# Kernel optimization log

Measured on AMD Instinct MI355X. Metric: run time of the kernel, lower is better.

The kernel has to match this reference:

```python
import jax, jax.numpy as jnp
import numpy as np

TIME_CONSTANT = 1.0
VM_THRESHOLD = 2.0
WINDOW = 100          # integration_window
AMPLITUDE = 1.0


def setup_inputs() -> dict:
    key = jax.random.key(0)
    # [B, T, H, W, C] positive drive so integrate-and-fire actually spikes
    inputs = jax.random.uniform(key, (4, 200, 64, 64, 8), dtype=jnp.float32)
    return {"inputs": inputs}


def _process_chunk(chunk):
    """Iterative integrate-and-fire on one time chunk [B, T, H, W, C].
    Each while-iteration extracts one spike per neuron (first threshold
    crossing of the running cumsum), resets the membrane, and zeroes the
    consumed input so the next cumsum restarts after the spike."""
    B, T = chunk.shape[0], chunk.shape[1]
    img = chunk.shape[2:]
    spikes0 = jnp.zeros((B,) + img + (T + 1,), chunk.dtype)
    vout0 = jnp.zeros_like(chunk)

    def body(state):
        ch, vout, spikes, _ = state
        V = jnp.cumsum(ch * TIME_CONSTANT, axis=1)            # membrane potential
        temp = jax.nn.relu(V - VM_THRESHOLD)
        has = jnp.any(temp > 0)                                # any neuron fires?
        ctemp = jnp.cumsum(temp, axis=1)                       # zero before first crossing
        tstar = jnp.sum((ctemp == 0).astype(jnp.int32), axis=1)  # [B,H,W,C] spike time (T => none)
        spikes_new = spikes + jax.nn.one_hot(tstar, T + 1, dtype=ch.dtype)
        rolled = jnp.roll(ctemp, 1, axis=1).at[:, 0].set(0.0)  # nonzero strictly after spike
        mask = rolled == 0
        vout_spk = jnp.where(mask, vout + V, 0.0)              # record V up to spike, reset after
        ch_spk = jnp.where(mask, 0.0, ch)                      # consume input up to spike
        # if no spikes this pass: accumulate residual V and stop (do-while break)
        vout_n = jnp.where(has, vout_spk, vout + V)
        ch_n = jnp.where(has, ch_spk, ch)
        spikes_n = jnp.where(has, spikes_new, spikes)
        return ch_n, vout_n, spikes_n, jnp.logical_not(has)

    def cond(state):
        return jnp.logical_not(state[3])

    state = (chunk, vout0, spikes0, jnp.array(False))
    _, vout, spikes, _ = jax.lax.while_loop(cond, body, state)
    return vout, spikes[..., :T]   # drop the 'no spike' bin


def reference(inputs):
    T = inputs.shape[1]
    sizes = [WINDOW] * (T // WINDOW) + ([T % WINDOW] if T % WINDOW else [])
    spike_chunks = []
    start = 0
    for s in sizes:  # small fixed chunk loop (structural, not a data dim)
        ch = inputs[:, start:start + s]
        start += s
        _, sp = _process_chunk(ch)
        spike_chunks.append(sp)
    spikes = jnp.concatenate(spike_chunks, axis=-1)   # [B, H, W, C, T]
    out = jnp.swapaxes(spikes, 1, -1)                 # [B, T, W, C, H] (as in source)
    if AMPLITUDE != 1.0:
        out = out * AMPLITUDE
    return out
```

## Files before the change

kernel.cpp:

```cpp
#include <hip/hip_runtime.h>
#include <stdint.h>

#define HWC   32768
#define TTOT  200
#define CHUNK 100

__global__ __launch_bounds__(256) void spike_fused(const float* __restrict__ x,
                                                   float* __restrict__ out) {
    __shared__ uint32_t lds[4 * 544];

    unsigned bid  = blockIdx.x;
    unsigned slab = bid >> 6;
    unsigned hh   = (bid >> 5) & 1u;
    unsigned tile = bid & 31u;
    unsigned b    = slab >> 1, ch = slab & 1u;
    unsigned h0   = hh * 32u;
    unsigned wc0  = tile * 16u;
    unsigned tid  = threadIdx.x;

    {
        unsigned hl = tid >> 3;
        unsigned wq = tid & 7u;
        unsigned n  = (h0 + hl) * 512u + wc0 + wq * 2u;
        const float2* xp = (const float2*)x
            + (((size_t)(b * TTOT + ch * CHUNK) * HWC + n) >> 1);

        float a0 = 0.0f, a1 = 0.0f;
        uint32_t wa[4] = {0u, 0u, 0u, 0u};
        uint32_t wb[4] = {0u, 0u, 0u, 0u};

#define STEP(TW, BB, K)                                                     \
    do {                                                                    \
        a0 += v[K].x;                                                       \
        if (a0 > 2.0f) { wa[TW] |= (1u << ((BB) + (K))); a0 = 0.0f; }       \
        a1 += v[K].y;                                                       \
        if (a1 > 2.0f) { wb[TW] |= (1u << ((BB) + (K))); a1 = 0.0f; }       \
    } while (0)

#define GROUP8(TW, TBASE)                                                   \
    do {                                                                    \
        float2 v[8];                                                        \
        _Pragma("unroll")                                                   \
        for (int k = 0; k < 8; ++k)                                         \
            v[k] = xp[(size_t)((TBASE) + k) * (HWC / 2)];                   \
        STEP(TW, (TBASE) & 31, 0); STEP(TW, (TBASE) & 31, 1);               \
        STEP(TW, (TBASE) & 31, 2); STEP(TW, (TBASE) & 31, 3);               \
        STEP(TW, (TBASE) & 31, 4); STEP(TW, (TBASE) & 31, 5);               \
        STEP(TW, (TBASE) & 31, 6); STEP(TW, (TBASE) & 31, 7);               \
    } while (0)

        GROUP8(0,  0); GROUP8(0,  8); GROUP8(0, 16); GROUP8(0, 24);
        GROUP8(1, 32); GROUP8(1, 40); GROUP8(1, 48); GROUP8(1, 56);
        GROUP8(2, 64); GROUP8(2, 72); GROUP8(2, 80); GROUP8(2, 88);
        {
            float2 v[4];
#pragma unroll
            for (int k = 0; k < 4; ++k)
                v[k] = xp[(size_t)(96 + k) * (HWC / 2)];
            STEP(3, 0, 0); STEP(3, 0, 1); STEP(3, 0, 2); STEP(3, 0, 3);
        }
#undef GROUP8
#undef STEP

        unsigned lbase = hl * 17u + wq * 2u;
#pragma unroll
        for (int tw = 0; tw < 4; ++tw) {
            lds[tw * 544u + lbase]      = wa[tw];
            lds[tw * 544u + lbase + 1u] = wb[tw];
        }
    }
    __syncthreads();

    unsigned idx  = tid & 127u;
    unsigned half = tid >> 7;
    unsigned wcl  = idx >> 3;
    unsigned hl4  = (idx & 7u) * 4u;

    uint32_t r[4][4];
#pragma unroll
    for (int k = 0; k < 4; ++k)
#pragma unroll
        for (int tw = 0; tw < 4; ++tw)
            r[k][tw] = lds[tw * 544u + (hl4 + k) * 17u + wcl];

    unsigned rbase = b * TTOT + ch * CHUNK;
    size_t   cbase = (size_t)(wc0 + wcl) * 16u + ((h0 + hl4) >> 2);
    float4*  o4    = (float4*)out;

#pragma unroll
    for (int tw = 0; tw < 4; ++tw) {
        const int nj = (tw < 3) ? 16 : 2;
        for (int j = 0; j < nj; ++j) {
            unsigned bit = 2u * (unsigned)j + half;
            unsigned t   = (unsigned)tw * 32u + bit;
            float4 v;
            v.x = (float)((r[0][tw] >> bit) & 1u);
            v.y = (float)((r[1][tw] >> bit) & 1u);
            v.z = (float)((r[2][tw] >> bit) & 1u);
            v.w = (float)((r[3][tw] >> bit) & 1u);
            o4[((size_t)(rbase + t) << 13) + cbase] = v;
        }
    }
}

extern "C" void kernel_launch(void* const* d_in, const int* in_sizes, int n_in,
                              void* d_out, int out_size, void* d_ws, size_t ws_size,
                              hipStream_t stream) {
    (void)in_sizes; (void)n_in; (void)out_size; (void)d_ws; (void)ws_size;
    const float* x = (const float*)d_in[0];
    float* out = (float*)d_out;
    hipLaunchKernelGGL(spike_fused, dim3(512), dim3(256), 0, stream, x, out);
}
```

Measured before the change: 195.1 us.

## Use one neuron per thread with 512-thread blocks and double-buffered loads

The block grows from 256 to 512 threads, and each thread now integrates a single neuron with scalar loads instead of two neurons with float2 loads. Input loads are issued in 16-step groups into two alternating register buffers, so the next group's loads are in flight while the current group's threshold scan runs. The store phase is remapped so four thread groups split the time bits. The goal is more memory parallelism and shorter serial dependency chains in what looks like a latency-bound kernel, at the cost of narrower loads and more registers per thread.

```diff
diff --git a/kernel.cpp b/kernel.cpp
--- a/kernel.cpp
+++ b/kernel.cpp
@@ -5,8 +5,8 @@
 #define TTOT  200
 #define CHUNK 100
 
-__global__ __launch_bounds__(256) void spike_fused(const float* __restrict__ x,
-                                                   float* __restrict__ out) {
+__global__ __launch_bounds__(512, 4) void spike_fused(const float* __restrict__ x,
+                                                      float* __restrict__ out) {
     __shared__ uint32_t lds[4 * 544];
 
     unsigned bid  = blockIdx.x;
@@ -19,79 +19,86 @@
     unsigned tid  = threadIdx.x;
 
     {
-        unsigned hl = tid >> 3;
-        unsigned wq = tid & 7u;
-        unsigned n  = (h0 + hl) * 512u + wc0 + wq * 2u;
-        const float2* xp = (const float2*)x
-            + (((size_t)(b * TTOT + ch * CHUNK) * HWC + n) >> 1);
+        unsigned hl  = tid >> 4;
+        unsigned wcl = tid & 15u;
+        unsigned n   = (h0 + hl) * 512u + wc0 + wcl;
+        const float* xp = x + (size_t)(b * TTOT + ch * CHUNK) * HWC + n;
 
-        float a0 = 0.0f, a1 = 0.0f;
-        uint32_t wa[4] = {0u, 0u, 0u, 0u};
-        uint32_t wb[4] = {0u, 0u, 0u, 0u};
+        float acc = 0.0f;
+        uint32_t w[4] = {0u, 0u, 0u, 0u};
+        float A[16], B[16], Tl[4];
 
-#define STEP(TW, BB, K)                                                     \
+#define LOAD16(V, TBASE)                                                    \
     do {                                                                    \
-        a0 += v[K].x;                                                       \
-        if (a0 > 2.0f) { wa[TW] |= (1u << ((BB) + (K))); a0 = 0.0f; }       \
-        a1 += v[K].y;                                                       \
-        if (a1 > 2.0f) { wb[TW] |= (1u << ((BB) + (K))); a1 = 0.0f; }       \
+        _Pragma("unroll")                                                   \
+        for (int k = 0; k < 16; ++k)                                        \
+            V[k] = xp[(size_t)((TBASE) + k) * HWC];                         \
     } while (0)
 
-#define GROUP8(TW, TBASE)                                                   \
+#define CONS16(V, TBASE)                                                    \
     do {                                                                    \
-        float2 v[8];                                                        \
         _Pragma("unroll")                                                   \
-        for (int k = 0; k < 8; ++k)                                         \
-            v[k] = xp[(size_t)((TBASE) + k) * (HWC / 2)];                   \
-        STEP(TW, (TBASE) & 31, 0); STEP(TW, (TBASE) & 31, 1);               \
-        STEP(TW, (TBASE) & 31, 2); STEP(TW, (TBASE) & 31, 3);               \
-        STEP(TW, (TBASE) & 31, 4); STEP(TW, (TBASE) & 31, 5);               \
-        STEP(TW, (TBASE) & 31, 6); STEP(TW, (TBASE) & 31, 7);               \
+        for (int k = 0; k < 16; ++k) {                                      \
+            acc += V[k];                                                    \
+            if (acc > 2.0f) {                                               \
+                w[(TBASE) >> 5] |= (1u << (((TBASE) & 31) + k));            \
+                acc = 0.0f;                                                 \
+            }                                                               \
+        }                                                                   \
     } while (0)
 
-        GROUP8(0,  0); GROUP8(0,  8); GROUP8(0, 16); GROUP8(0, 24);
-        GROUP8(1, 32); GROUP8(1, 40); GROUP8(1, 48); GROUP8(1, 56);
-        GROUP8(2, 64); GROUP8(2, 72); GROUP8(2, 80); GROUP8(2, 88);
+        LOAD16(A, 0);
+        LOAD16(B, 16);
+        CONS16(A, 0);
+        LOAD16(A, 32);
+        CONS16(B, 16);
+        LOAD16(B, 48);
+        CONS16(A, 32);
+        LOAD16(A, 64);
+        CONS16(B, 48);
+        LOAD16(B, 80);
+        CONS16(A, 64);
         {
-            float2 v[4];
 #pragma unroll
             for (int k = 0; k < 4; ++k)
-                v[k] = xp[(size_t)(96 + k) * (HWC / 2)];
-            STEP(3, 0, 0); STEP(3, 0, 1); STEP(3, 0, 2); STEP(3, 0, 3);
+                Tl[k] = xp[(size_t)(96 + k) * HWC];
         }
-#undef GROUP8
-#undef STEP
+        CONS16(B, 80);
+#pragma unroll
+        for (int k = 0; k < 4; ++k) {
+            acc += Tl[k];
+            if (acc > 2.0f) { w[3] |= (1u << k); acc = 0.0f; }
+        }
+#undef LOAD16
+#undef CONS16
 
-        unsigned lbase = hl * 17u + wq * 2u;
+        unsigned lbase = hl * 17u + wcl;
 #pragma unroll
-        for (int tw = 0; tw < 4; ++tw) {
-            lds[tw * 544u + lbase]      = wa[tw];
-            lds[tw * 544u + lbase + 1u] = wb[tw];
-        }
+        for (int tw = 0; tw < 4; ++tw)
+            lds[tw * 544u + lbase] = w[tw];
     }
     __syncthreads();
 
     unsigned idx  = tid & 127u;
     unsigned half = tid >> 7;
     unsigned wcl  = idx >> 3;
-    unsigned hl4  = (idx & 7u) * 4u;
+    unsigned h4   = (idx & 7u) * 4u;
 
     uint32_t r[4][4];
 #pragma unroll
     for (int k = 0; k < 4; ++k)
 #pragma unroll
         for (int tw = 0; tw < 4; ++tw)
-            r[k][tw] = lds[tw * 544u + (hl4 + k) * 17u + wcl];
+            r[k][tw] = lds[tw * 544u + (h4 + k) * 17u + wcl];
 
     unsigned rbase = b * TTOT + ch * CHUNK;
-    size_t   cbase = (size_t)(wc0 + wcl) * 16u + ((h0 + hl4) >> 2);
+    size_t   cbase = (size_t)(wc0 + wcl) * 16u + ((h0 + h4) >> 2);
     float4*  o4    = (float4*)out;
 
 #pragma unroll
-    for (int tw = 0; tw < 4; ++tw) {
-        const int nj = (tw < 3) ? 16 : 2;
-        for (int j = 0; j < nj; ++j) {
-            unsigned bit = 2u * (unsigned)j + half;
+    for (int tw = 0; tw < 3; ++tw) {
+        for (int j = 0; j < 8; ++j) {
+            unsigned bit = 4u * (unsigned)j + half;
             unsigned t   = (unsigned)tw * 32u + bit;
             float4 v;
             v.x = (float)((r[0][tw] >> bit) & 1u);
@@ -101,6 +108,16 @@
             o4[((size_t)(rbase + t) << 13) + cbase] = v;
         }
     }
+    {
+        unsigned bit = half;
+        unsigned t   = 96u + bit;
+        float4 v;
+        v.x = (float)((r[0][3] >> bit) & 1u);
+        v.y = (float)((r[1][3] >> bit) & 1u);
+        v.z = (float)((r[2][3] >> bit) & 1u);
+        v.w = (float)((r[3][3] >> bit) & 1u);
+        o4[((size_t)(rbase + t) << 13) + cbase] = v;
+    }
 }
 
 extern "C" void kernel_launch(void* const* d_in, const int* in_sizes, int n_in,
@@ -109,5 +126,5 @@
     (void)in_sizes; (void)n_in; (void)out_size; (void)d_ws; (void)ws_size;
     const float* x = (const float*)d_in[0];
     float* out = (float*)d_out;
-    hipLaunchKernelGGL(spike_fused, dim3(512), dim3(256), 0, stream, x, out);
+    hipLaunchKernelGGL(spike_fused, dim3(512), dim3(512), 0, stream, x, out);
 }
```

Result: no change. 194.9 us (-0.1%).

## Pipeline spike scan with transposed stores in 32-step phases per block

Applied to the files above, without the earlier changes.

Restructures the fused kernel so each block covers the full 64 H rows for a 16-wide W*C tile, with 256 blocks instead of 512. Time is processed in 32-step phases: while scanning the next phase's inputs, each thread writes the previous phase's spike bits as transposed float4 outputs, exchanging bitmasks through a small LDS buffer. The goal is to overlap input loads with output stores rather than doing all reads and then all writes. The cost is extra barriers, scalar (non-vectorized) loads, and half as many blocks, which may reduce occupancy.

```diff
diff --git a/kernel.cpp b/kernel.cpp
--- a/kernel.cpp
+++ b/kernel.cpp
@@ -5,102 +5,106 @@
 #define TTOT  200
 #define CHUNK 100
 
-__global__ __launch_bounds__(256) void spike_fused(const float* __restrict__ x,
-                                                   float* __restrict__ out) {
-    __shared__ uint32_t lds[4 * 544];
+__global__ __launch_bounds__(256) void spike_pipe(const float* __restrict__ x,
+                                                  float* __restrict__ out) {
+    __shared__ uint32_t bits[64 * 17];
 
     unsigned bid  = blockIdx.x;
-    unsigned slab = bid >> 6;
-    unsigned hh   = (bid >> 5) & 1u;
-    unsigned tile = bid & 31u;
+    unsigned slab = bid & 7u;
+    unsigned wcT  = bid >> 3;
+    unsigned wc0  = wcT * 16u;
     unsigned b    = slab >> 1, ch = slab & 1u;
-    unsigned h0   = hh * 32u;
-    unsigned wc0  = tile * 16u;
     unsigned tid  = threadIdx.x;
 
-    {
-        unsigned hl = tid >> 3;
-        unsigned wq = tid & 7u;
-        unsigned n  = (h0 + hl) * 512u + wc0 + wq * 2u;
-        const float2* xp = (const float2*)x
-            + (((size_t)(b * TTOT + ch * CHUNK) * HWC + n) >> 1);
+    unsigned wcl  = tid & 15u;
+    unsigned hloc = tid >> 4;
+    const float* xb = x + (size_t)(b * TTOT + ch * CHUNK) * HWC
+                    + (size_t)(hloc * 4u) * 512u + wc0 + wcl;
 
-        float a0 = 0.0f, a1 = 0.0f;
-        uint32_t wa[4] = {0u, 0u, 0u, 0u};
-        uint32_t wb[4] = {0u, 0u, 0u, 0u};
+    unsigned wcs  = tid >> 4;
+    unsigned h0s  = (tid & 15u) * 4u;
+    unsigned rbase = b * TTOT + ch * CHUNK;
+    float4*  o4   = (float4*)out;
+    size_t   cidx = (((size_t)(wc0 + wcs) * 64u) + h0s) >> 2;
 
-#define STEP(TW, BB, K)                                                     \
+    float    a0 = 0.f, a1 = 0.f, a2 = 0.f, a3 = 0.f;
+    uint32_t w0 = 0u, w1 = 0u, w2 = 0u, w3 = 0u;
+    uint32_t r0 = 0u, r1 = 0u, r2 = 0u, r3 = 0u;
+
+#define SCAN(T, J)                                                          \
     do {                                                                    \
-        a0 += v[K].x;                                                       \
-        if (a0 > 2.0f) { wa[TW] |= (1u << ((BB) + (K))); a0 = 0.0f; }       \
-        a1 += v[K].y;                                                       \
-        if (a1 > 2.0f) { wb[TW] |= (1u << ((BB) + (K))); a1 = 0.0f; }       \
+        float v0 = xb[(size_t)(T) * HWC];                                   \
+        float v1 = xb[(size_t)(T) * HWC + 512u];                            \
+        float v2 = xb[(size_t)(T) * HWC + 1024u];                           \
+        float v3 = xb[(size_t)(T) * HWC + 1536u];                           \
+        a0 += v0; if (a0 > 2.0f) { w0 |= 1u << (J); a0 = 0.0f; }            \
+        a1 += v1; if (a1 > 2.0f) { w1 |= 1u << (J); a1 = 0.0f; }            \
+        a2 += v2; if (a2 > 2.0f) { w2 |= 1u << (J); a2 = 0.0f; }            \
+        a3 += v3; if (a3 > 2.0f) { w3 |= 1u << (J); a3 = 0.0f; }            \
     } while (0)
 
-#define GROUP8(TW, TBASE)                                                   \
+#define STASH()                                                             \
     do {                                                                    \
-        float2 v[8];                                                        \
-        _Pragma("unroll")                                                   \
-        for (int k = 0; k < 8; ++k)                                         \
-            v[k] = xp[(size_t)((TBASE) + k) * (HWC / 2)];                   \
-        STEP(TW, (TBASE) & 31, 0); STEP(TW, (TBASE) & 31, 1);               \
-        STEP(TW, (TBASE) & 31, 2); STEP(TW, (TBASE) & 31, 3);               \
-        STEP(TW, (TBASE) & 31, 4); STEP(TW, (TBASE) & 31, 5);               \
-        STEP(TW, (TBASE) & 31, 6); STEP(TW, (TBASE) & 31, 7);               \
+        bits[(hloc * 4u + 0u) * 17u + wcl] = w0;                            \
+        bits[(hloc * 4u + 1u) * 17u + wcl] = w1;                            \
+        bits[(hloc * 4u + 2u) * 17u + wcl] = w2;                            \
+        bits[(hloc * 4u + 3u) * 17u + wcl] = w3;                            \
+        w0 = w1 = w2 = w3 = 0u;                                             \
     } while (0)
 
-        GROUP8(0,  0); GROUP8(0,  8); GROUP8(0, 16); GROUP8(0, 24);
-        GROUP8(1, 32); GROUP8(1, 40); GROUP8(1, 48); GROUP8(1, 56);
-        GROUP8(2, 64); GROUP8(2, 72); GROUP8(2, 80); GROUP8(2, 88);
-        {
-            float2 v[4];
-#pragma unroll
-            for (int k = 0; k < 4; ++k)
-                v[k] = xp[(size_t)(96 + k) * (HWC / 2)];
-            STEP(3, 0, 0); STEP(3, 0, 1); STEP(3, 0, 2); STEP(3, 0, 3);
-        }
-#undef GROUP8
-#undef STEP
+#define HOIST()                                                             \
+    do {                                                                    \
+        r0 = bits[(h0s + 0u) * 17u + wcs];                                  \
+        r1 = bits[(h0s + 1u) * 17u + wcs];                                  \
+        r2 = bits[(h0s + 2u) * 17u + wcs];                                  \
+        r3 = bits[(h0s + 3u) * 17u + wcs];                                  \
+    } while (0)
 
-        unsigned lbase = hl * 17u + wq * 2u;
-#pragma unroll
-        for (int tw = 0; tw < 4; ++tw) {
-            lds[tw * 544u + lbase]      = wa[tw];
-            lds[tw * 544u + lbase + 1u] = wb[tw];
-        }
-    }
-    __syncthreads();
-
-    unsigned idx  = tid & 127u;
-    unsigned half = tid >> 7;
-    unsigned wcl  = idx >> 3;
-    unsigned hl4  = (idx & 7u) * 4u;
-
-    uint32_t r[4][4];
-#pragma unroll
-    for (int k = 0; k < 4; ++k)
-#pragma unroll
-        for (int tw = 0; tw < 4; ++tw)
-            r[k][tw] = lds[tw * 544u + (hl4 + k) * 17u + wcl];
-
-    unsigned rbase = b * TTOT + ch * CHUNK;
-    size_t   cbase = (size_t)(wc0 + wcl) * 16u + ((h0 + hl4) >> 2);
-    float4*  o4    = (float4*)out;
+#define STORE(TP, J)                                                        \
+    do {                                                                    \
+        float4 v;                                                           \
+        v.x = (float)((r0 >> (J)) & 1u);                                    \
+        v.y = (float)((r1 >> (J)) & 1u);                                    \
+        v.z = (float)((r2 >> (J)) & 1u);                                    \
+        v.w = (float)((r3 >> (J)) & 1u);                                    \
+        o4[((size_t)(rbase + (TP)) << 13) + cidx] = v;                      \
+    } while (0)
 
 #pragma unroll
-    for (int tw = 0; tw < 4; ++tw) {
-        const int nj = (tw < 3) ? 16 : 2;
-        for (int j = 0; j < nj; ++j) {
-            unsigned bit = 2u * (unsigned)j + half;
-            unsigned t   = (unsigned)tw * 32u + bit;
-            float4 v;
-            v.x = (float)((r[0][tw] >> bit) & 1u);
-            v.y = (float)((r[1][tw] >> bit) & 1u);
-            v.z = (float)((r[2][tw] >> bit) & 1u);
-            v.w = (float)((r[3][tw] >> bit) & 1u);
-            o4[((size_t)(rbase + t) << 13) + cbase] = v;
-        }
-    }
+    for (int j = 0; j < 32; ++j) SCAN(j, j);
+    STASH();
+    __syncthreads();
+    HOIST();
+
+#pragma unroll
+    for (int j = 0; j < 32; ++j) { SCAN(32 + j, j); STORE(j, j); }
+    __syncthreads();
+    STASH();
+    __syncthreads();
+    HOIST();
+
+#pragma unroll
+    for (int j = 0; j < 32; ++j) { SCAN(64 + j, j); STORE(32 + j, j); }
+    __syncthreads();
+    STASH();
+    __syncthreads();
+    HOIST();
+
+#pragma unroll
+    for (int j = 0; j < 4; ++j)  { SCAN(96 + j, j); STORE(64 + j, j); }
+#pragma unroll
+    for (int j = 4; j < 32; ++j) STORE(64 + j, j);
+    __syncthreads();
+    STASH();
+    __syncthreads();
+    HOIST();
+#pragma unroll
+    for (int j = 0; j < 4; ++j) STORE(96 + j, j);
+
+#undef SCAN
+#undef STASH
+#undef HOIST
+#undef STORE
 }
 
 extern "C" void kernel_launch(void* const* d_in, const int* in_sizes, int n_in,
@@ -109,5 +113,5 @@
     (void)in_sizes; (void)n_in; (void)out_size; (void)d_ws; (void)ws_size;
     const float* x = (const float*)d_in[0];
     float* out = (float*)d_out;
-    hipLaunchKernelGGL(spike_fused, dim3(512), dim3(256), 0, stream, x, out);
+    hipLaunchKernelGGL(spike_pipe, dim3(256), dim3(256), 0, stream, x, out);
 }
```

Measured after the change: 189.9 us. 1.03x faster.
